# Kernel tuning notes

Hardware: AMD Instinct MI355X
Metric: run time of the kernel (lower is better)

The kernel has to match this reference:

```python
import jax, jax.numpy as jnp
import numpy as np

USER_NUM, ITEM_NUM, EMB, R = 8192, 16384, 32, 3

def setup_inputs() -> dict:
    key = jax.random.key(0)
    k1, k2, k3 = jax.random.split(key, 3)
    # Xavier-uniform-like embeddings
    u_lim = (6.0 / (USER_NUM + EMB)) ** 0.5
    i_lim = (6.0 / (ITEM_NUM + EMB)) ** 0.5
    user_emb = jax.random.uniform(k1, (USER_NUM, EMB), jnp.float32, -u_lim, u_lim)
    item_emb = jax.random.uniform(k2, (ITEM_NUM, EMB), jnp.float32, -i_lim, i_lim)
    # Densified normalized link-propagation matrix (user x item).
    # Scale ~1/item_num so repeated propagation stays numerically tame,
    # mimicking the degree-normalized product in __init__.
    sparse_norm = jax.random.uniform(k3, (USER_NUM, ITEM_NUM), jnp.float32) * (2.0 / ITEM_NUM)
    return {"user_emb": user_emb, "item_emb": item_emb, "sparse_norm": sparse_norm}

def reference(user_emb, item_emb, sparse_norm):
    # LinkProp forward (t == 0.0 branch): r rounds of cross propagation,
    # then mean over the (r+1) layer outputs. Running sums avoid stacking.
    u_k, i_k = user_emb, item_emb
    u_sum, i_sum = user_emb, item_emb
    for _ in range(R):
        u_next = sparse_norm @ i_k          # [U, d]
        i_next = sparse_norm.T @ u_k        # [I, d]
        u_sum = u_sum + u_next
        i_sum = i_sum + i_next
        u_k, i_k = u_next, i_next
    inv = 1.0 / (R + 1)
    return (u_sum * inv, i_sum * inv)
```

## Files before the change

### kernel.cpp

```cpp
#include <hip/hip_runtime.h>

#define U_N 8192
#define I_N 16384

typedef float f4 __attribute__((ext_vector_type(4)));
typedef unsigned long long u64;

#if defined(__has_builtin)
#if __has_builtin(__builtin_amdgcn_cvt_pk_fp8_f32)
#define HAS_HW_FP8 1
#endif
#endif
#ifndef HAS_HW_FP8
#define HAS_HW_FP8 0
#endif

__device__ __forceinline__ unsigned char f2e4m3_soft(float x) {
  unsigned char sign = (x < 0.f) ? 0x80 : 0x00;
  float ax = fabsf(x);
  unsigned char code;
  if (ax >= 448.f) {
    code = 0x7E;
  } else if (ax < 0.015625f) {
    int q = (int)rintf(ax * 512.f);
    code = (unsigned char)q;
  } else {
    int e; float f = frexpf(ax, &e);
    int q = (int)rintf(f * 16.f);
    if (q == 16) { q = 8; e += 1; }
    code = (unsigned char)(((e + 6) << 3) | (q - 8));
  }
  return sign | code;
}

__device__ __forceinline__ unsigned char q8(float x) {
#if HAS_HW_FP8
  return (unsigned char)(__builtin_amdgcn_cvt_pk_fp8_f32(x, 0.f, 0, false) & 0xff);
#else
  return f2e4m3_soft(x);
#endif
}

__device__ __forceinline__ unsigned int pack4_fp8(float a, float b, float c, float d) {
#if HAS_HW_FP8
  int v = __builtin_amdgcn_cvt_pk_fp8_f32(a, b, 0, false);
  v = __builtin_amdgcn_cvt_pk_fp8_f32(c, d, v, true);
  return (unsigned int)v;
#else
  return (unsigned)f2e4m3_soft(a) | ((unsigned)f2e4m3_soft(b) << 8) |
         ((unsigned)f2e4m3_soft(c) << 16) | ((unsigned)f2e4m3_soft(d) << 24);
#endif
}

#define SCALE_S   131072.f
#define SCALE_V0  512.f
#define SCALE_VK  65536.f

__global__ __launch_bounds__(256)
void convert_kernel(const float* __restrict__ Sf,
                    const float* __restrict__ u0,
                    const float* __restrict__ i0,
                    unsigned char* __restrict__ S8,
                    unsigned char* __restrict__ S8T,
                    unsigned char* __restrict__ wT0,
                    unsigned char* __restrict__ vT0)
{
  const int tid = threadIdx.x;
  const int bid = blockIdx.x;
  if (bid < 1024) {
    const int idx = bid * 256 + tid;
    wT0[(idx & 31) * U_N + (idx >> 5)] = q8(u0[idx] * SCALE_V0);
  } else if (bid < 3072) {
    const int idx = (bid - 1024) * 256 + tid;
    vT0[(idx & 31) * I_N + (idx >> 5)] = q8(i0[idx] * SCALE_V0);
  } else {
    __shared__ unsigned char lds[64 * 68];
    const int b = bid - 3072;
    const int tr = b >> 8;
    const int tc = b & 255;
    const int mr = (tid >> 4) << 2;
    const int mc = (tid & 15) << 2;
    const size_t base = ((size_t)tr * 64 + mr) * I_N + (size_t)tc * 64 + mc;
    float fs[4][4];
#pragma unroll
    for (int i = 0; i < 4; ++i) {
      float4 f = *(const float4*)(Sf + base + (size_t)i * I_N);
      fs[i][0] = f.x * SCALE_S; fs[i][1] = f.y * SCALE_S;
      fs[i][2] = f.z * SCALE_S; fs[i][3] = f.w * SCALE_S;
    }
#pragma unroll
    for (int i = 0; i < 4; ++i)
      *(unsigned int*)&S8[base + (size_t)i * I_N] =
          pack4_fp8(fs[i][0], fs[i][1], fs[i][2], fs[i][3]);
#pragma unroll
    for (int j = 0; j < 4; ++j)
      *(unsigned int*)&lds[(mc + j) * 68 + mr] =
          pack4_fp8(fs[0][j], fs[1][j], fs[2][j], fs[3][j]);
    __syncthreads();
    const int c = tid >> 2;
    const int s = (tid & 3) << 4;
    uint4 v;
    v.x = *(const unsigned int*)&lds[c * 68 + s];
    v.y = *(const unsigned int*)&lds[c * 68 + s + 4];
    v.z = *(const unsigned int*)&lds[c * 68 + s + 8];
    v.w = *(const unsigned int*)&lds[c * 68 + s + 12];
    *(uint4*)&S8T[((size_t)tc * 64 + c) * U_N + (size_t)tr * 64 + s] = v;
  }
}

__device__ __forceinline__ void half_gemm(
    const unsigned char* __restrict__ A,
    const unsigned char* __restrict__ Bt,
    float* __restrict__ part,
    unsigned char* smem,
    int rgroup, int ksplit, int nrows, size_t kdim, float descale, int tid)
{
  const int lane = tid & 63;
  const int wave = tid >> 6;
  const int m = lane & 15;
  const int quad = lane >> 4;
  const int r0 = rgroup * 64 + wave * 16;
  const int kbase = ksplit * 2048;
  f4 acc0 = {0.f, 0.f, 0.f, 0.f};
  f4 acc1 = {0.f, 0.f, 0.f, 0.f};
  for (int ch = 0; ch < 4; ++ch) {
    const int kb = kbase + ch * 512;
#pragma unroll
    for (int it = 0; it < 4; ++it) {
      const int idx = it * 256 + tid;
      const int e = idx >> 5;
      const int o = (idx & 31) * 16;
      *(uint4*)&smem[e * 528 + o] = *(const uint4*)&Bt[(size_t)e * kdim + kb + o];
    }
    __syncthreads();
#pragma unroll
    for (int kk = 0; kk < 512; kk += 32) {
      const long a  = *(const long*)(A + (size_t)(r0 + m) * kdim + kb + kk + quad * 8);
      const long b0 = *(const long*)&smem[m * 528 + kk + quad * 8];
      const long b1 = *(const long*)&smem[(m + 16) * 528 + kk + quad * 8];
      acc0 = __builtin_amdgcn_mfma_f32_16x16x32_fp8_fp8(a, b0, acc0, 0, 0, 0);
      acc1 = __builtin_amdgcn_mfma_f32_16x16x32_fp8_fp8(a, b1, acc1, 0, 0, 0);
    }
    __syncthreads();
  }
  float* dst = part + (size_t)ksplit * ((size_t)nrows * 32);
#pragma unroll
  for (int i2 = 0; i2 < 4; ++i2) {
    const int r = r0 + quad * 4 + i2;
    dst[r * 32 + m]      = acc0[i2] * descale;
    dst[r * 32 + 16 + m] = acc1[i2] * descale;
  }
}

__global__ __launch_bounds__(256, 4)
void pass_kernel(const unsigned char* __restrict__ S8,
                 const unsigned char* __restrict__ S8T,
                 const unsigned char* __restrict__ vT,
                 const unsigned char* __restrict__ wT,
                 float* __restrict__ u_part,
                 float* __restrict__ i_part,
                 float descale)
{
  __shared__ unsigned char smem[16896];
  const int bid = blockIdx.x;
  if (bid < 1024) {
    half_gemm(S8, vT, u_part, smem, bid & 127, bid >> 7, U_N, (size_t)I_N,
              descale, threadIdx.x);
  } else {
    const int b = bid - 1024;
    half_gemm(S8T, wT, i_part, smem, b & 255, b >> 8, I_N, (size_t)U_N,
              descale, threadIdx.x);
  }
}

__global__ __launch_bounds__(256, 4)
void pass_fallback(const float* __restrict__ Sf,
                   const unsigned char* __restrict__ vT,
                   const unsigned char* __restrict__ wT,
                   float* __restrict__ u_part,
                   float* __restrict__ i_part,
                   float descale)
{
  __shared__ unsigned char smem[16896];
  const int tid = threadIdx.x;
  const int lane = tid & 63;
  const int wave = tid >> 6;
  const int m = lane & 15;
  const int quad = lane >> 4;
  const int bid = blockIdx.x;

  if (bid < 1024) {
    const int rg = bid & 127, ks = bid >> 7;
    const int r0 = rg * 64 + wave * 16;
    const int cbase = ks * 2048;
    f4 acc0 = {0.f, 0.f, 0.f, 0.f};
    f4 acc1 = {0.f, 0.f, 0.f, 0.f};
    for (int ch = 0; ch < 4; ++ch) {
      const int cb = cbase + ch * 512;
#pragma unroll
      for (int it = 0; it < 4; ++it) {
        const int idx = it * 256 + tid;
        const int e = idx >> 5;
        const int o = (idx & 31) * 16;
        *(uint4*)&smem[e * 528 + o] = *(const uint4*)&vT[(size_t)e * I_N + cb + o];
      }
      __syncthreads();
#pragma unroll
      for (int kk = 0; kk < 512; kk += 32) {
        const float* p = Sf + (size_t)(r0 + m) * I_N + cb + kk + quad * 8;
        u64 av = 0;
#pragma unroll
        for (int j = 0; j < 8; ++j) av |= (u64)q8(p[j] * SCALE_S) << (8 * j);
        const long a = (long)av;
        const long b0 = *(const long*)&smem[m * 528 + kk + quad * 8];
        const long b1 = *(const long*)&smem[(m + 16) * 528 + kk + quad * 8];
        acc0 = __builtin_amdgcn_mfma_f32_16x16x32_fp8_fp8(a, b0, acc0, 0, 0, 0);
        acc1 = __builtin_amdgcn_mfma_f32_16x16x32_fp8_fp8(a, b1, acc1, 0, 0, 0);
      }
      __syncthreads();
    }
    float* dst = u_part + (size_t)ks * (U_N * 32);
#pragma unroll
    for (int i2 = 0; i2 < 4; ++i2) {
      const int r = r0 + quad * 4 + i2;
      dst[r * 32 + m]      = acc0[i2] * descale;
      dst[r * 32 + 16 + m] = acc1[i2] * descale;
    }
  } else {
    const int b = bid - 1024;
    const int cg = b & 255, rs = b >> 8;
    const int c0 = cg * 64;
    const int rbase = rs * 2048;
    const int cw = wave * 16;
    unsigned char* stile = smem;
    unsigned char* wlds  = smem + 9216;
    f4 acc0 = {0.f, 0.f, 0.f, 0.f};
    f4 acc1 = {0.f, 0.f, 0.f, 0.f};
    for (int ch = 0; ch < 16; ++ch) {
      const int rb = rbase + ch * 128;
#pragma unroll
      for (int it = 0; it < 4; ++it) {
        const int idx = it * 256 + tid;
        const int rr = idx >> 3;
        const int o = (idx & 7) * 8;
        const float* p = Sf + (size_t)(rb + rr) * I_N + c0 + o;
        u64 v = 0;
#pragma unroll
        for (int j = 0; j < 8; ++j) v |= (u64)q8(p[j] * SCALE_S) << (8 * j);
        *(u64*)&stile[rr * 72 + o] = v;
      }
      {
        const int e = tid >> 3;
        const int o = (tid & 7) * 16;
        *(uint4*)&wlds[e * 144 + o] = *(const uint4*)&wT[(size_t)e * U_N + rb + o];
      }
      __syncthreads();
#pragma unroll
      for (int kk = 0; kk < 128; kk += 32) {
        u64 av = 0;
#pragma unroll
        for (int j = 0; j < 8; ++j)
          av |= (u64)stile[(kk + quad * 8 + j) * 72 + cw + m] << (8 * j);
        const long b0 = *(const long*)&wlds[m * 144 + kk + quad * 8];
        const long b1 = *(const long*)&wlds[(m + 16) * 144 + kk + quad * 8];
        acc0 = __builtin_amdgcn_mfma_f32_16x16x32_fp8_fp8((long)av, b0, acc0, 0, 0, 0);
        acc1 = __builtin_amdgcn_mfma_f32_16x16x32_fp8_fp8((long)av, b1, acc1, 0, 0, 0);
      }
      __syncthreads();
    }
    float* dst = i_part + (size_t)rs * (I_N * 32);
#pragma unroll
    for (int i2 = 0; i2 < 4; ++i2) {
      const int c = c0 + cw + quad * 4 + i2;
      dst[c * 32 + m]      = acc0[i2] * descale;
      dst[c * 32 + 16 + m] = acc1[i2] * descale;
    }
  }
}

__global__ __launch_bounds__(256)
void reduce_kernel(const float* __restrict__ u_part, const float* __restrict__ i_part,
                   const float* __restrict__ u0, const float* __restrict__ i0,
                   float* __restrict__ acc_u, float* __restrict__ acc_i,
                   unsigned char* __restrict__ wT, unsigned char* __restrict__ vT,
                   float* __restrict__ out_u, float* __restrict__ out_i,
                   int round)
{
  const int gid = blockIdx.x * 256 + threadIdx.x;
  if (gid < U_N * 32) {
    float s = 0.f;
#pragma unroll
    for (int sp = 0; sp < 8; ++sp) s += u_part[(size_t)sp * (U_N * 32) + gid];
    if (round == 1)      acc_u[gid] = u0[gid] + s;
    else if (round == 2) acc_u[gid] += s;
    else                 out_u[gid] = (acc_u[gid] + s) * 0.25f;
    if (round < 3) wT[(gid & 31) * U_N + (gid >> 5)] = q8(s * SCALE_VK);
  } else {
    const int g = gid - U_N * 32;
    float s = 0.f;
#pragma unroll
    for (int sp = 0; sp < 4; ++sp) s += i_part[(size_t)sp * (I_N * 32) + g];
    if (round == 1)      acc_i[g] = i0[g] + s;
    else if (round == 2) acc_i[g] += s;
    else                 out_i[g] = (acc_i[g] + s) * 0.25f;
    if (round < 3) vT[(g & 31) * I_N + (g >> 5)] = q8(s * SCALE_VK);
  }
}

extern "C" void kernel_launch(void* const* d_in, const int* in_sizes, int n_in,
                              void* d_out, int out_size, void* d_ws, size_t ws_size,
                              hipStream_t stream) {
  const float* u0 = (const float*)d_in[0];
  const float* i0 = (const float*)d_in[1];
  const float* Sf = (const float*)d_in[2];
  float* out_u = (float*)d_out;
  float* out_i = out_u + U_N * 32;
  unsigned char* ws = (unsigned char*)d_ws;

  const size_t S8_BYTES = (size_t)U_N * I_N;
  const size_t SMALL_BYTES = 20709376;
  const bool f8 = ws_size >= 2 * S8_BYTES + SMALL_BYTES;

  unsigned char* S8 = nullptr;
  unsigned char* S8T = nullptr;
  unsigned char* cur;
  if (f8) { S8 = ws; S8T = ws + S8_BYTES; cur = ws + 2 * S8_BYTES; }
  else    { cur = ws; }
  float* u_part = (float*)cur;
  float* i_part = u_part + 8 * U_N * 32;
  float* acc_u  = i_part + 4 * I_N * 32;
  float* acc_i  = acc_u + U_N * 32;
  unsigned char* wT = (unsigned char*)(acc_i + I_N * 32);
  unsigned char* vT = wT + 32 * U_N;

  convert_kernel<<<f8 ? 35840 : 3072, 256, 0, stream>>>(Sf, u0, i0, S8, S8T, wT, vT);

  const float ds1 = 1.f / (SCALE_S * SCALE_V0);
  const float dsk = 1.f / (SCALE_S * SCALE_VK);
  for (int round = 1; round <= 3; ++round) {
    const float ds = (round == 1) ? ds1 : dsk;
    if (f8)
      pass_kernel<<<2048, 256, 0, stream>>>(S8, S8T, vT, wT, u_part, i_part, ds);
    else
      pass_fallback<<<2048, 256, 0, stream>>>(Sf, vT, wT, u_part, i_part, ds);
    reduce_kernel<<<3072, 256, 0, stream>>>(u_part, i_part, u0, i0, acc_u, acc_i,
                                            wT, vT, out_u, out_i, round);
  }
}
```

Before: 1.014 ms.

## Reschedule propagation into four sweeps sharing matrix reads across both chains

Exploits that the user and item recurrences form two independent chains, and interleaves them so each pass streams only S or S^T once while multiplying against up to 64 right-hand columns. This cuts the number of full fp8 matrix reads from six to four and widens A loads to 16 bytes. Reductions are split into per-stage kernels that also emit the quantized vectors for the next sweep. The sweeps are more serialized, with fewer blocks per launch and additional kernel launches.

```diff
diff --git a/kernel.cpp b/kernel.cpp
--- a/kernel.cpp
+++ b/kernel.cpp
@@ -5,6 +5,7 @@
 
 typedef float f4 __attribute__((ext_vector_type(4)));
 typedef unsigned long long u64;
+typedef unsigned char u8;
 
 #if defined(__has_builtin)
 #if __has_builtin(__builtin_amdgcn_cvt_pk_fp8_f32)
@@ -60,19 +61,19 @@
 void convert_kernel(const float* __restrict__ Sf,
                     const float* __restrict__ u0,
                     const float* __restrict__ i0,
-                    unsigned char* __restrict__ S8,
-                    unsigned char* __restrict__ S8T,
-                    unsigned char* __restrict__ wT0,
-                    unsigned char* __restrict__ vT0)
+                    u8* __restrict__ S8,
+                    u8* __restrict__ S8T,
+                    u8* __restrict__ wT0,
+                    u8* __restrict__ vT0)
 {
   const int tid = threadIdx.x;
   const int bid = blockIdx.x;
   if (bid < 1024) {
     const int idx = bid * 256 + tid;
-    wT0[(idx & 31) * U_N + (idx >> 5)] = q8(u0[idx] * SCALE_V0);
+    wT0[(size_t)(idx & 31) * U_N + (idx >> 5)] = q8(u0[idx] * SCALE_V0);
   } else if (bid < 3072) {
     const int idx = (bid - 1024) * 256 + tid;
-    vT0[(idx & 31) * I_N + (idx >> 5)] = q8(i0[idx] * SCALE_V0);
+    vT0[(size_t)(idx & 31) * I_N + (idx >> 5)] = q8(i0[idx] * SCALE_V0);
   } else {
     __shared__ unsigned char lds[64 * 68];
     const int b = bid - 3072;
@@ -108,25 +109,32 @@
   }
 }
 
-__device__ __forceinline__ void half_gemm(
-    const unsigned char* __restrict__ A,
-    const unsigned char* __restrict__ Bt,
-    float* __restrict__ part,
-    unsigned char* smem,
-    int rgroup, int ksplit, int nrows, size_t kdim, float descale, int tid)
-{
-  const int lane = tid & 63;
-  const int wave = tid >> 6;
-  const int m = lane & 15;
-  const int quad = lane >> 4;
+union B16 { uint4 v; long l[2]; };
+
+template <int NE>
+__global__ __launch_bounds__(256, 4)
+void sweep_kernel(const u8* __restrict__ A, const u8* __restrict__ Bt,
+                  float* __restrict__ part, int rg_mask, int rg_shift,
+                  int nrows, int kdim, float ds_lo, float ds_hi)
+{
+  __shared__ u8 smem[NE * 528];
+  const int tid = threadIdx.x;
+  const int lane = tid & 63, wave = tid >> 6;
+  const int m = lane & 15, quad = lane >> 4;
+  const int bid = blockIdx.x;
+  const int rgroup = bid & rg_mask, ksplit = bid >> rg_shift;
   const int r0 = rgroup * 64 + wave * 16;
   const int kbase = ksplit * 2048;
-  f4 acc0 = {0.f, 0.f, 0.f, 0.f};
-  f4 acc1 = {0.f, 0.f, 0.f, 0.f};
+  f4 acc[NE / 16];
+#pragma unroll
+  for (int eb = 0; eb < NE / 16; ++eb) acc[eb] = {0.f, 0.f, 0.f, 0.f};
+
+  const u8* arow = A + (size_t)(r0 + m) * kdim;
+
   for (int ch = 0; ch < 4; ++ch) {
     const int kb = kbase + ch * 512;
 #pragma unroll
-    for (int it = 0; it < 4; ++it) {
+    for (int it = 0; it < NE / 8; ++it) {
       const int idx = it * 256 + tid;
       const int e = idx >> 5;
       const int o = (idx & 31) * 16;
@@ -134,49 +142,91 @@
     }
     __syncthreads();
 #pragma unroll
-    for (int kk = 0; kk < 512; kk += 32) {
-      const long a  = *(const long*)(A + (size_t)(r0 + m) * kdim + kb + kk + quad * 8);
-      const long b0 = *(const long*)&smem[m * 528 + kk + quad * 8];
-      const long b1 = *(const long*)&smem[(m + 16) * 528 + kk + quad * 8];
-      acc0 = __builtin_amdgcn_mfma_f32_16x16x32_fp8_fp8(a, b0, acc0, 0, 0, 0);
-      acc1 = __builtin_amdgcn_mfma_f32_16x16x32_fp8_fp8(a, b1, acc1, 0, 0, 0);
+    for (int pr = 0; pr < 8; ++pr) {
+      B16 av;
+      av.v = *(const uint4*)(arow + kb + pr * 64 + quad * 16);
+#pragma unroll
+      for (int eb = 0; eb < NE / 16; ++eb) {
+        B16 bv;
+        bv.v = *(const uint4*)&smem[(m + eb * 16) * 528 + pr * 64 + quad * 16];
+        acc[eb] = __builtin_amdgcn_mfma_f32_16x16x32_fp8_fp8(av.l[0], bv.l[0], acc[eb], 0, 0, 0);
+        acc[eb] = __builtin_amdgcn_mfma_f32_16x16x32_fp8_fp8(av.l[1], bv.l[1], acc[eb], 0, 0, 0);
+      }
     }
     __syncthreads();
   }
-  float* dst = part + (size_t)ksplit * ((size_t)nrows * 32);
-#pragma unroll
-  for (int i2 = 0; i2 < 4; ++i2) {
-    const int r = r0 + quad * 4 + i2;
-    dst[r * 32 + m]      = acc0[i2] * descale;
-    dst[r * 32 + 16 + m] = acc1[i2] * descale;
-  }
-}
-
-__global__ __launch_bounds__(256, 4)
-void pass_kernel(const unsigned char* __restrict__ S8,
-                 const unsigned char* __restrict__ S8T,
-                 const unsigned char* __restrict__ vT,
-                 const unsigned char* __restrict__ wT,
-                 float* __restrict__ u_part,
-                 float* __restrict__ i_part,
-                 float descale)
-{
-  __shared__ unsigned char smem[16896];
-  const int bid = blockIdx.x;
-  if (bid < 1024) {
-    half_gemm(S8, vT, u_part, smem, bid & 127, bid >> 7, U_N, (size_t)I_N,
-              descale, threadIdx.x);
-  } else {
-    const int b = bid - 1024;
-    half_gemm(S8T, wT, i_part, smem, b & 255, b >> 8, I_N, (size_t)U_N,
-              descale, threadIdx.x);
-  }
+  float* dst = part + (size_t)ksplit * ((size_t)nrows * NE);
+#pragma unroll
+  for (int eb = 0; eb < NE / 16; ++eb) {
+    const float ds = (eb < 2) ? ds_lo : ds_hi;
+#pragma unroll
+    for (int i2 = 0; i2 < 4; ++i2) {
+      const int r = r0 + quad * 4 + i2;
+      dst[(size_t)r * NE + eb * 16 + m] = acc[eb][i2] * ds;
+    }
+  }
+}
+
+__global__ __launch_bounds__(256)
+void reduce_uA(const float* __restrict__ u_part, const float* __restrict__ u0,
+               float* __restrict__ acc_u, u8* __restrict__ wT64)
+{
+  const int gid = blockIdx.x * 256 + threadIdx.x;
+  float s = 0.f;
+#pragma unroll
+  for (int sp = 0; sp < 8; ++sp) s += u_part[(size_t)sp * (U_N * 32) + gid];
+  acc_u[gid] = u0[gid] + s;
+  wT64[(size_t)(32 + (gid & 31)) * U_N + (gid >> 5)] = q8(s * SCALE_VK);
+}
+
+__global__ __launch_bounds__(256)
+void reduce_iB(const float* __restrict__ i_part, const float* __restrict__ i0,
+               float* __restrict__ acc_i, u8* __restrict__ vT64)
+{
+  const int gid = blockIdx.x * 256 + threadIdx.x;
+  const int c = gid >> 5, e = gid & 31;
+  float s1 = 0.f, s2 = 0.f;
+#pragma unroll
+  for (int sp = 0; sp < 4; ++sp) {
+    s1 += i_part[(size_t)sp * (I_N * 64) + (size_t)c * 64 + e];
+    s2 += i_part[(size_t)sp * (I_N * 64) + (size_t)c * 64 + 32 + e];
+  }
+  acc_i[gid] = i0[gid] + s1 + s2;
+  vT64[(size_t)e * I_N + c]        = q8(s1 * SCALE_VK);
+  vT64[(size_t)(32 + e) * I_N + c] = q8(s2 * SCALE_VK);
+}
+
+__global__ __launch_bounds__(256)
+void reduce_uC(const float* __restrict__ u_part, const float* __restrict__ acc_u,
+               float* __restrict__ out_u, u8* __restrict__ wT2)
+{
+  const int gid = blockIdx.x * 256 + threadIdx.x;
+  const int r = gid >> 5, e = gid & 31;
+  float s2 = 0.f, s3 = 0.f;
+#pragma unroll
+  for (int sp = 0; sp < 8; ++sp) {
+    s2 += u_part[(size_t)sp * (U_N * 64) + (size_t)r * 64 + e];
+    s3 += u_part[(size_t)sp * (U_N * 64) + (size_t)r * 64 + 32 + e];
+  }
+  out_u[gid] = (acc_u[gid] + s2 + s3) * 0.25f;
+  wT2[(size_t)e * U_N + r] = q8(s2 * SCALE_VK);
+}
+
+__global__ __launch_bounds__(256)
+void reduce_iD(const float* __restrict__ i_part, const float* __restrict__ acc_i,
+               float* __restrict__ out_i)
+{
+  const int gid = blockIdx.x * 256 + threadIdx.x;
+  float s = 0.f;
+#pragma unroll
+  for (int sp = 0; sp < 4; ++sp) s += i_part[(size_t)sp * (I_N * 32) + gid];
+  out_i[gid] = (acc_i[gid] + s) * 0.25f;
 }
 
 __global__ __launch_bounds__(256, 4)
 void pass_fallback(const float* __restrict__ Sf,
-                   const unsigned char* __restrict__ vT,
-                   const unsigned char* __restrict__ wT,
+                   const u8* __restrict__ vT,
+                   const u8* __restrict__ wT,
                    float* __restrict__ u_part,
                    float* __restrict__ i_part,
                    float descale)
@@ -279,12 +329,12 @@
 }
 
 __global__ __launch_bounds__(256)
-void reduce_kernel(const float* __restrict__ u_part, const float* __restrict__ i_part,
-                   const float* __restrict__ u0, const float* __restrict__ i0,
-                   float* __restrict__ acc_u, float* __restrict__ acc_i,
-                   unsigned char* __restrict__ wT, unsigned char* __restrict__ vT,
-                   float* __restrict__ out_u, float* __restrict__ out_i,
-                   int round)
+void reduce_fallback(const float* __restrict__ u_part, const float* __restrict__ i_part,
+                     const float* __restrict__ u0, const float* __restrict__ i0,
+                     float* __restrict__ acc_u, float* __restrict__ acc_i,
+                     u8* __restrict__ wT, u8* __restrict__ vT,
+                     float* __restrict__ out_u, float* __restrict__ out_i,
+                     int round)
 {
   const int gid = blockIdx.x * 256 + threadIdx.x;
   if (gid < U_N * 32) {
@@ -315,35 +365,59 @@
   const float* Sf = (const float*)d_in[2];
   float* out_u = (float*)d_out;
   float* out_i = out_u + U_N * 32;
-  unsigned char* ws = (unsigned char*)d_ws;
-
-  const size_t S8_BYTES = (size_t)U_N * I_N;
-  const size_t SMALL_BYTES = 20709376;
-  const bool f8 = ws_size >= 2 * S8_BYTES + SMALL_BYTES;
-
-  unsigned char* S8 = nullptr;
-  unsigned char* S8T = nullptr;
-  unsigned char* cur;
-  if (f8) { S8 = ws; S8T = ws + S8_BYTES; cur = ws + 2 * S8_BYTES; }
-  else    { cur = ws; }
-  float* u_part = (float*)cur;
-  float* i_part = u_part + 8 * U_N * 32;
-  float* acc_u  = i_part + 4 * I_N * 32;
-  float* acc_i  = acc_u + U_N * 32;
-  unsigned char* wT = (unsigned char*)(acc_i + I_N * 32);
-  unsigned char* vT = wT + 32 * U_N;
-
-  convert_kernel<<<f8 ? 35840 : 3072, 256, 0, stream>>>(Sf, u0, i0, S8, S8T, wT, vT);
-
-  const float ds1 = 1.f / (SCALE_S * SCALE_V0);
+  u8* ws = (u8*)d_ws;
+
+  const size_t S8B = (size_t)U_N * I_N;
+  const size_t FULL_BYTES = 2 * S8B
+      + (size_t)8 * U_N * 64 * 4 + (size_t)4 * I_N * 64 * 4
+      + (size_t)U_N * 32 * 4 + (size_t)I_N * 32 * 4
+      + (size_t)64 * U_N + (size_t)64 * I_N
+      + (size_t)32 * I_N + (size_t)32 * U_N;
+  const bool f8 = ws_size >= FULL_BYTES;
+
+  const float dsA = 1.f / (SCALE_S * SCALE_V0);
   const float dsk = 1.f / (SCALE_S * SCALE_VK);
-  for (int round = 1; round <= 3; ++round) {
-    const float ds = (round == 1) ? ds1 : dsk;
-    if (f8)
-      pass_kernel<<<2048, 256, 0, stream>>>(S8, S8T, vT, wT, u_part, i_part, ds);
-    else
+
+  if (f8) {
+    u8* S8  = ws;
+    u8* S8T = ws + S8B;
+    float* u_part = (float*)(ws + 2 * S8B);
+    float* i_part = u_part + (size_t)8 * U_N * 64;
+    float* acc_u  = i_part + (size_t)4 * I_N * 64;
+    float* acc_i  = acc_u + U_N * 32;
+    u8* wT64 = (u8*)(acc_i + I_N * 32);
+    u8* vT64 = wT64 + (size_t)64 * U_N;
+    u8* vT0  = vT64 + (size_t)64 * I_N;
+    u8* wT2  = vT0 + (size_t)32 * I_N;
+
+    convert_kernel<<<35840, 256, 0, stream>>>(Sf, u0, i0, S8, S8T, wT64, vT0);
+
+    sweep_kernel<32><<<1024, 256, 0, stream>>>(S8, vT0, u_part, 127, 7,
+                                               U_N, I_N, dsA, dsA);
+    reduce_uA<<<1024, 256, 0, stream>>>(u_part, u0, acc_u, wT64);
+    sweep_kernel<64><<<1024, 256, 0, stream>>>(S8T, wT64, i_part, 255, 8,
+                                               I_N, U_N, dsA, dsk);
+    reduce_iB<<<2048, 256, 0, stream>>>(i_part, i0, acc_i, vT64);
+    sweep_kernel<64><<<1024, 256, 0, stream>>>(S8, vT64, u_part, 127, 7,
+                                               U_N, I_N, dsk, dsk);
+    reduce_uC<<<1024, 256, 0, stream>>>(u_part, acc_u, out_u, wT2);
+    sweep_kernel<32><<<1024, 256, 0, stream>>>(S8T, wT2, i_part, 255, 8,
+                                               I_N, U_N, dsk, dsk);
+    reduce_iD<<<2048, 256, 0, stream>>>(i_part, acc_i, out_i);
+  } else {
+    float* u_part = (float*)ws;
+    float* i_part = u_part + 8 * U_N * 32;
+    float* acc_u  = i_part + 4 * I_N * 32;
+    float* acc_i  = acc_u + U_N * 32;
+    u8* wT = (u8*)(acc_i + I_N * 32);
+    u8* vT = wT + 32 * U_N;
+
+    convert_kernel<<<3072, 256, 0, stream>>>(Sf, u0, i0, nullptr, nullptr, wT, vT);
+    for (int round = 1; round <= 3; ++round) {
+      const float ds = (round == 1) ? dsA : dsk;
       pass_fallback<<<2048, 256, 0, stream>>>(Sf, vT, wT, u_part, i_part, ds);
-    reduce_kernel<<<3072, 256, 0, stream>>>(u_part, i_part, u0, i0, acc_u, acc_i,
-                                            wT, vT, out_u, out_i, round);
-  }
-}
+      reduce_fallback<<<3072, 256, 0, stream>>>(u_part, i_part, u0, i0, acc_u, acc_i,
+                                                wT, vT, out_u, out_i, round);
+    }
+  }
+}
```

Result: faster. 921.6 us (-9.2%).
